# Performance work log

Hardware: AMD Instinct MI355X
Metric: run time of the kernel (lower is better)

Reference implementation:

```python
import jax, jax.numpy as jnp
import numpy as np

N_REF, PHRASE_LEN, ASCII = 50000, 32, 128
BATCH = 16


def setup_inputs() -> dict:
    key = jax.random.key(0)
    k1, k2 = jax.random.split(key)
    x = jax.random.normal(k1, (BATCH, PHRASE_LEN, ASCII), dtype=jnp.float32)
    raw_phrases = jax.random.normal(k2, (N_REF, PHRASE_LEN, ASCII), dtype=jnp.float32)
    return {"x": x, "raw_phrases": raw_phrases}


def reference(x, raw_phrases):
    # dist[b, n] = sum_{l,a} (raw_phrases[n,l,a] - x[b,l,a])**2
    # Expanded form avoids materializing the [B, N, L, A] difference tensor
    # (which would be ~13 GB); exact same math up to fp reassociation.
    r2 = jnp.sum(raw_phrases * raw_phrases, axis=(1, 2))          # [N]
    x2 = jnp.sum(x * x, axis=(1, 2))                              # [B]
    xr = jnp.einsum('bla,nla->bn', x, raw_phrases)                # [B, N]
    dist = r2[None, :] - 2.0 * xr + x2[:, None]                   # [B, N]
    # torch F.softmax on a 1-D tensor (no dim) softmaxes over the reference axis.
    # Note: the original applies softmax to the (positive) distances directly.
    return jax.nn.softmax(dist, axis=-1)                          # [B, N]
```

## Files before the change

### kernel.cpp

```cpp
#include <hip/hip_runtime.h>
#include <math.h>

#define N_REF   50000
#define BATCH   16
#define KDIM    4096
#define CHUNK   256
#define NCHUNK  (KDIM / CHUNK)
#define RPB     16
#define RPW     4

typedef __attribute__((address_space(3))) uint32_t lds_u32;
typedef const __attribute__((address_space(1))) uint32_t glb_u32;

__global__ __launch_bounds__(256) void dist_kernel(const float* __restrict__ x,
                                                   const float* __restrict__ raw,
                                                   float* __restrict__ dist)
{
    __shared__ float xs[2][BATCH * CHUNK];
    const int tid  = threadIdx.x;
    const int lane = tid & 63;
    const int wv   = tid >> 6;
    const long n_base = (long)blockIdx.x * RPB + (long)wv * RPW;

    float acc[BATCH][RPW];
    #pragma unroll
    for (int b = 0; b < BATCH; ++b)
        #pragma unroll
        for (int r = 0; r < RPW; ++r) acc[b][r] = 0.f;
    float r2a[RPW] = {0.f, 0.f, 0.f, 0.f};
    float4 rv[RPW];

#define STAGE(buf, c) do {                                                      \
        _Pragma("unroll")                                                       \
        for (int i_ = 0; i_ < 4; ++i_) {                                        \
            const int b_ = i_ * 4 + wv;                                         \
            const float* g_ = x + (size_t)b_ * KDIM + (size_t)(c) * CHUNK + lane * 4; \
            const float* l_ = &xs[buf][b_ * CHUNK];                             \
            __builtin_amdgcn_global_load_lds((glb_u32*)g_, (lds_u32*)l_, 16, 0, 0); \
        }                                                                       \
    } while (0)

#define LOADRV(c) do {                                                          \
        _Pragma("unroll")                                                       \
        for (int r_ = 0; r_ < RPW; ++r_)                                        \
            rv[r_] = *(const float4*)(raw + (size_t)(n_base + r_) * KDIM        \
                                          + (size_t)(c) * CHUNK + lane * 4);    \
    } while (0)

#define COMPUTE(buf) do {                                                       \
        _Pragma("unroll")                                                       \
        for (int r_ = 0; r_ < RPW; ++r_) {                                      \
            r2a[r_] = fmaf(rv[r_].x, rv[r_].x, r2a[r_]);                        \
            r2a[r_] = fmaf(rv[r_].y, rv[r_].y, r2a[r_]);                        \
            r2a[r_] = fmaf(rv[r_].z, rv[r_].z, r2a[r_]);                        \
            r2a[r_] = fmaf(rv[r_].w, rv[r_].w, r2a[r_]);                        \
        }                                                                       \
        _Pragma("unroll")                                                       \
        for (int b_ = 0; b_ < BATCH; ++b_) {                                    \
            const float4 xv_ = *(const float4*)(&xs[buf][b_ * CHUNK + lane * 4]); \
            _Pragma("unroll")                                                   \
            for (int r_ = 0; r_ < RPW; ++r_) {                                  \
                acc[b_][r_] = fmaf(rv[r_].x, xv_.x, acc[b_][r_]);               \
                acc[b_][r_] = fmaf(rv[r_].y, xv_.y, acc[b_][r_]);               \
                acc[b_][r_] = fmaf(rv[r_].z, xv_.z, acc[b_][r_]);               \
                acc[b_][r_] = fmaf(rv[r_].w, xv_.w, acc[b_][r_]);               \
            }                                                                   \
        }                                                                       \
    } while (0)

    STAGE(0, 0);
    __syncthreads();

    int buf = 0;
    #pragma unroll 1
    for (int c = 0; c < NCHUNK - 1; ++c) {
        LOADRV(c);
        STAGE(buf ^ 1, c + 1);
        COMPUTE(buf);
        __syncthreads();
        buf ^= 1;
    }
    LOADRV(NCHUNK - 1);
    COMPUTE(buf);

    float vals[64];
    #pragma unroll
    for (int b = 0; b < BATCH; ++b)
        #pragma unroll
        for (int r = 0; r < RPW; ++r) vals[b * RPW + r] = acc[b][r];

    #pragma unroll
    for (int k = 0; k < 6; ++k) {
        const int bit = 1 << k;
        const bool hi = (lane & bit) != 0;
        #pragma unroll
        for (int i = 0; i < (64 >> (k + 1)); ++i) {
            const float a  = vals[2 * i];
            const float bb = vals[2 * i + 1];
            const float keep = hi ? bb : a;
            const float send = hi ? a  : bb;
            const float recv = __shfl_xor(send, bit, 64);
            vals[i] = keep + recv;
        }
    }

    #pragma unroll
    for (int r = 0; r < RPW; ++r) {
        #pragma unroll
        for (int k = 0; k < 6; ++k)
            r2a[r] += __shfl_xor(r2a[r], 1 << k, 64);
    }

    const int b_out = lane >> 2;
    const int r_out = lane & 3;
    const float r2v = (r_out == 0) ? r2a[0] : (r_out == 1) ? r2a[1]
                    : (r_out == 2) ? r2a[2] : r2a[3];
    dist[(size_t)b_out * N_REF + (size_t)(n_base + r_out)] = r2v - 2.0f * vals[0];
}

#define SMB   25
#define SMC   2000

__global__ __launch_bounds__(256) void softmax_part(const float* __restrict__ d,
                                                    float2* __restrict__ part)
{
    const int row = blockIdx.y, cb = blockIdx.x;
    const float* p = d + (size_t)row * N_REF + (size_t)cb * SMC;
    const int tid = threadIdx.x;

    float m = -INFINITY, s = 0.f;
    #pragma unroll
    for (int i = 0; i < 2; ++i) {
        const int q = tid + i * 256;
        if (q < SMC / 4) {
            const float4 v = *(const float4*)(p + q * 4);
            const float M = fmaxf(m, fmaxf(fmaxf(v.x, v.y), fmaxf(v.z, v.w)));
            s = s * __expf(m - M) + __expf(v.x - M) + __expf(v.y - M)
                                  + __expf(v.z - M) + __expf(v.w - M);
            m = M;
        }
    }
    #pragma unroll
    for (int k = 1; k < 64; k <<= 1) {
        const float mo = __shfl_xor(m, k, 64);
        const float so = __shfl_xor(s, k, 64);
        const float M  = fmaxf(m, mo);
        s = s * __expf(m - M) + so * __expf(mo - M);
        m = M;
    }
    __shared__ float2 wsum[4];
    const int wv = tid >> 6, lane = tid & 63;
    if (lane == 0) wsum[wv] = make_float2(m, s);
    __syncthreads();
    if (tid == 0) {
        float M = wsum[0].x, S = wsum[0].y;
        #pragma unroll
        for (int i = 1; i < 4; ++i) {
            const float M2 = fmaxf(M, wsum[i].x);
            S = S * __expf(M - M2) + wsum[i].y * __expf(wsum[i].x - M2);
            M = M2;
        }
        part[row * SMB + cb] = make_float2(M, S);
    }
}

__global__ __launch_bounds__(256) void softmax_norm(float* __restrict__ d,
                                                    const float2* __restrict__ part)
{
    const int row = blockIdx.y, cb = blockIdx.x;
    const int tid = threadIdx.x;

    float M = -INFINITY, S = 0.f;
    #pragma unroll
    for (int i = 0; i < SMB; ++i) {
        const float2 ps = part[row * SMB + i];
        const float M2 = fmaxf(M, ps.x);
        S = S * __expf(M - M2) + ps.y * __expf(ps.x - M2);
        M = M2;
    }
    const float Sinv = 1.f / S;

    float* p = d + (size_t)row * N_REF + (size_t)cb * SMC;
    #pragma unroll
    for (int i = 0; i < 2; ++i) {
        const int q = tid + i * 256;
        if (q < SMC / 4) {
            float4 v = *(float4*)(p + q * 4);
            v.x = __expf(v.x - M) * Sinv;
            v.y = __expf(v.y - M) * Sinv;
            v.z = __expf(v.z - M) * Sinv;
            v.w = __expf(v.w - M) * Sinv;
            *(float4*)(p + q * 4) = v;
        }
    }
}

extern "C" void kernel_launch(void* const* d_in, const int* in_sizes, int n_in,
                              void* d_out, int out_size, void* d_ws, size_t ws_size,
                              hipStream_t stream) {
    const float* x   = (const float*)d_in[0];
    const float* raw = (const float*)d_in[1];
    float* out = (float*)d_out;
    float2* part = (float2*)d_ws;

    dist_kernel<<<N_REF / RPB, 256, 0, stream>>>(x, raw, out);
    softmax_part<<<dim3(SMB, BATCH), 256, 0, stream>>>(out, part);
    softmax_norm<<<dim3(SMB, BATCH), 256, 0, stream>>>(out, part);
}
```

Baseline: 191.2 us.

## Double-buffer raw-phrase register loads and relax barrier wait counts

Splits the raw-phrase registers into two sets so the next chunk's global loads are issued before computing the current chunk. The chunk loop is unrolled by two to ping-pong both the register sets and the LDS buffers. The block-wide sync is replaced with a partial vmcnt wait plus s_barrier, so the outstanding raw loads are not drained at each barrier. This aims to keep more memory requests in flight to hide global latency. The cost is extra VGPRs, which may reduce occupancy.

```diff
diff --git a/kernel.cpp b/kernel.cpp
--- a/kernel.cpp
+++ b/kernel.cpp
@@ -28,7 +28,7 @@
         #pragma unroll
         for (int r = 0; r < RPW; ++r) acc[b][r] = 0.f;
     float r2a[RPW] = {0.f, 0.f, 0.f, 0.f};
-    float4 rv[RPW];
+    float4 rvA[RPW], rvB[RPW];
 
 #define STAGE(buf, c) do {                                                      \
         _Pragma("unroll")                                                       \
@@ -40,21 +40,14 @@
         }                                                                       \
     } while (0)
 
-#define LOADRV(c) do {                                                          \
+#define LOADRV(dst, c) do {                                                     \
         _Pragma("unroll")                                                       \
         for (int r_ = 0; r_ < RPW; ++r_)                                        \
-            rv[r_] = *(const float4*)(raw + (size_t)(n_base + r_) * KDIM        \
-                                          + (size_t)(c) * CHUNK + lane * 4);    \
-    } while (0)
-
-#define COMPUTE(buf) do {                                                       \
-        _Pragma("unroll")                                                       \
-        for (int r_ = 0; r_ < RPW; ++r_) {                                      \
-            r2a[r_] = fmaf(rv[r_].x, rv[r_].x, r2a[r_]);                        \
-            r2a[r_] = fmaf(rv[r_].y, rv[r_].y, r2a[r_]);                        \
-            r2a[r_] = fmaf(rv[r_].z, rv[r_].z, r2a[r_]);                        \
-            r2a[r_] = fmaf(rv[r_].w, rv[r_].w, r2a[r_]);                        \
-        }                                                                       \
+            dst[r_] = *(const float4*)(raw + (size_t)(n_base + r_) * KDIM       \
+                                           + (size_t)(c) * CHUNK + lane * 4);   \
+    } while (0)
+
+#define COMPUTE(rv, buf) do {                                                   \
         _Pragma("unroll")                                                       \
         for (int b_ = 0; b_ < BATCH; ++b_) {                                    \
             const float4 xv_ = *(const float4*)(&xs[buf][b_ * CHUNK + lane * 4]); \
@@ -66,22 +59,41 @@
                 acc[b_][r_] = fmaf(rv[r_].w, xv_.w, acc[b_][r_]);               \
             }                                                                   \
         }                                                                       \
+        _Pragma("unroll")                                                       \
+        for (int r_ = 0; r_ < RPW; ++r_) {                                      \
+            r2a[r_] = fmaf(rv[r_].x, rv[r_].x, r2a[r_]);                        \
+            r2a[r_] = fmaf(rv[r_].y, rv[r_].y, r2a[r_]);                        \
+            r2a[r_] = fmaf(rv[r_].z, rv[r_].z, r2a[r_]);                        \
+            r2a[r_] = fmaf(rv[r_].w, rv[r_].w, r2a[r_]);                        \
+        }                                                                       \
+    } while (0)
+
+#define PHASE_BARRIER() do {                                                    \
+        asm volatile("s_waitcnt vmcnt(4)" ::: "memory");                        \
+        __builtin_amdgcn_s_barrier();                                           \
+        __builtin_amdgcn_sched_barrier(0);                                      \
     } while (0)
 
     STAGE(0, 0);
-    __syncthreads();
-
-    int buf = 0;
+    LOADRV(rvA, 0);
+    PHASE_BARRIER();
+
     #pragma unroll 1
-    for (int c = 0; c < NCHUNK - 1; ++c) {
-        LOADRV(c);
-        STAGE(buf ^ 1, c + 1);
-        COMPUTE(buf);
-        __syncthreads();
-        buf ^= 1;
-    }
-    LOADRV(NCHUNK - 1);
-    COMPUTE(buf);
+    for (int cc = 0; cc < NCHUNK / 2 - 1; ++cc) {
+        STAGE(1, 2 * cc + 1);
+        LOADRV(rvB, 2 * cc + 1);
+        COMPUTE(rvA, 0);
+        PHASE_BARRIER();
+        STAGE(0, 2 * cc + 2);
+        LOADRV(rvA, 2 * cc + 2);
+        COMPUTE(rvB, 1);
+        PHASE_BARRIER();
+    }
+    STAGE(1, NCHUNK - 1);
+    LOADRV(rvB, NCHUNK - 1);
+    COMPUTE(rvA, 0);
+    PHASE_BARRIER();
+    COMPUTE(rvB, 1);
 
     float vals[64];
     #pragma unroll
```

After: 197.1 us. 3.1% more time.
